# Kernel optimization log

Measured on AMD Instinct MI355X. Metric: run time of the kernel, lower is better.

## Reference

```python
import jax, jax.numpy as jnp
import numpy as np

M = 10000      # spans with antecedents
KMAX = 30      # max antecedents per span
N = 12000      # total candidate spans (rows of g_i)
GDIM = 512     # span embedding dim
DDIM, GEDIM, SDIM = 20, 20, 20  # distance / genre / speaker embed dims
HID = 150      # Score hidden dim
GIJ = 3 * GDIM + DDIM + GEDIM + SDIM  # 1596
NDIST, NGENRE, NSPK = 10, 7, 3


def setup_inputs() -> dict:
    rng = np.random.default_rng(0)
    lengths = rng.integers(1, KMAX + 1, size=M)           # antecedents per span
    P = int(lengths.sum())
    seg_ids = np.repeat(np.arange(1, M + 1), lengths).astype(np.int32)  # segment 0 is the leading empty split
    pos_in_seg = np.concatenate([np.arange(l) for l in lengths]).astype(np.int32)
    seg_lengths = np.concatenate([[0], lengths]).astype(np.int32)        # [S], S = M+1
    mention_ids = rng.integers(0, N, size=P).astype(np.int32)
    antecedent_ids = rng.integers(0, N, size=P).astype(np.int32)
    dist_idx = rng.integers(0, NDIST, size=P).astype(np.int32)
    genre_idx = rng.integers(0, NGENRE, size=P).astype(np.int32)
    speaker_idx = rng.integers(0, NSPK, size=P).astype(np.int32)

    ks = jax.random.split(jax.random.key(0), 12)
    sc = lambda d: 1.0 / np.sqrt(d)
    return {
        'g_i': jax.random.normal(ks[0], (N, GDIM), jnp.float32),
        'mention_scores': jax.random.normal(ks[1], (N, 1), jnp.float32),
        'dist_emb': jax.random.normal(ks[2], (NDIST, DDIM), jnp.float32),
        'genre_emb': jax.random.normal(ks[3], (NGENRE, GEDIM), jnp.float32),
        'speaker_emb': jax.random.normal(ks[4], (NSPK, SDIM), jnp.float32),
        'W1': jax.random.normal(ks[5], (GIJ, HID), jnp.float32) * sc(GIJ),
        'b1': jnp.zeros((HID,), jnp.float32),
        'W2': jax.random.normal(ks[6], (HID, HID), jnp.float32) * sc(HID),
        'b2': jnp.zeros((HID,), jnp.float32),
        'W3': jax.random.normal(ks[7], (HID, 1), jnp.float32) * sc(HID),
        'b3': jnp.zeros((1,), jnp.float32),
        'mention_ids': jnp.asarray(mention_ids),
        'antecedent_ids': jnp.asarray(antecedent_ids),
        'dist_idx': jnp.asarray(dist_idx),
        'genre_idx': jnp.asarray(genre_idx),
        'speaker_idx': jnp.asarray(speaker_idx),
        'seg_ids': jnp.asarray(seg_ids),
        'pos_in_seg': jnp.asarray(pos_in_seg),
        'seg_lengths': jnp.asarray(seg_lengths),
    }


def reference(g_i, mention_scores, dist_emb, genre_emb, speaker_emb,
              W1, b1, W2, b2, W3, b3,
              mention_ids, antecedent_ids, dist_idx, genre_idx, speaker_idx,
              seg_ids, pos_in_seg, seg_lengths):
    # phi = cat(distance, genre, speaker) side features, [P, 60]
    phi = jnp.concatenate([dist_emb[dist_idx], genre_emb[genre_idx], speaker_emb[speaker_idx]], axis=1)
    i_g = g_i[mention_ids]      # [P, GDIM] irregular gather
    j_g = g_i[antecedent_ids]   # [P, GDIM]
    pairs = jnp.concatenate([i_g, j_g, i_g * j_g, phi], axis=1)  # [P, GIJ]
    # 3-layer MLP scorer (dropout is identity at inference)
    h = jax.nn.relu(pairs @ W1 + b1)
    h = jax.nn.relu(h @ W2 + b2)
    s_ij = (h @ W3 + b3)[:, 0]  # [P]
    coref = mention_scores[mention_ids, 0] + mention_scores[antecedent_ids, 0] + s_ij  # [P]
    # variable-length segment softmax with epsilon=0 appended, padded with 1000
    S = seg_lengths.shape[0]
    dense = jnp.full((S, KMAX + 1), -jnp.inf, jnp.float32)
    dense = dense.at[seg_ids, pos_in_seg].set(coref)
    dense = dense.at[jnp.arange(S), seg_lengths].set(0.0)  # epsilon slot
    probs = jax.nn.softmax(dense, axis=1)  # -inf slots -> 0
    col = jnp.arange(KMAX + 1)
    probs = jnp.where(col[None, :] > seg_lengths[:, None], 1000.0, probs)  # pad value 1000
    return probs  # [S, KMAX+1]
```

## Files before the change

kernel.cpp:

```cpp
#include <hip/hip_runtime.h>
#include <stdint.h>

#define GDIM   512
#define HID    150
#define HIDP   160
#define NROWS  12000
#define KP1    31
#define BM     128

typedef __attribute__((ext_vector_type(4))) float f32x4;
typedef __attribute__((ext_vector_type(2))) float f32x2;
typedef long i64;

__device__ __forceinline__ unsigned short f2bf(float x){
    unsigned int u = __float_as_uint(x);
    return (unsigned short)((u + 0x7fffu + ((u >> 16) & 1u)) >> 16);
}
__device__ __forceinline__ float bf2f(unsigned short u){
    return __uint_as_float(((unsigned int)u) << 16);
}
__device__ __forceinline__ i64 u2l(uint2 v){ return __builtin_bit_cast(i64, v); }
__device__ __forceinline__ f32x4 mfma8(i64 a, i64 b, f32x4 c){
    return __builtin_amdgcn_mfma_f32_16x16x32_fp8_fp8(a, b, c, 0, 0, 0);
}
__device__ __forceinline__ uint2 f8mulpk(uint2 m, uint2 a){
    f32x2 m0 = __builtin_amdgcn_cvt_pk_f32_fp8(m.x, false);
    f32x2 m1 = __builtin_amdgcn_cvt_pk_f32_fp8(m.x, true);
    f32x2 m2 = __builtin_amdgcn_cvt_pk_f32_fp8(m.y, false);
    f32x2 m3 = __builtin_amdgcn_cvt_pk_f32_fp8(m.y, true);
    f32x2 a0 = __builtin_amdgcn_cvt_pk_f32_fp8(a.x, false);
    f32x2 a1 = __builtin_amdgcn_cvt_pk_f32_fp8(a.x, true);
    f32x2 a2 = __builtin_amdgcn_cvt_pk_f32_fp8(a.y, false);
    f32x2 a3 = __builtin_amdgcn_cvt_pk_f32_fp8(a.y, true);
    unsigned int r0 = 0, r1 = 0;
    r0 = __builtin_amdgcn_cvt_pk_fp8_f32(m0[0]*a0[0], m0[1]*a0[1], r0, false);
    r0 = __builtin_amdgcn_cvt_pk_fp8_f32(m1[0]*a1[0], m1[1]*a1[1], r0, true);
    r1 = __builtin_amdgcn_cvt_pk_fp8_f32(m2[0]*a2[0], m2[1]*a2[1], r1, false);
    r1 = __builtin_amdgcn_cvt_pk_fp8_f32(m3[0]*a3[0], m3[1]*a3[1], r1, true);
    return (uint2){r0, r1};
}
__device__ __forceinline__ void glds16(const void* g, void* l){
    __builtin_amdgcn_global_load_lds(
        (const __attribute__((address_space(1))) unsigned int*)g,
        (__attribute__((address_space(3))) unsigned int*)l, 16, 0, 0);
}

__global__ void k_prep0(const float* __restrict__ g, unsigned char* __restrict__ g8,
                        int* __restrict__ hist, int4* __restrict__ recs,
                        const float* __restrict__ W1, unsigned char* __restrict__ W18,
                        const float* __restrict__ W2, unsigned char* __restrict__ W28, int P){
    int i = blockIdx.x * blockDim.x + threadIdx.x;
    if (i < NROWS) hist[i] = 0;
    if (i < BM) recs[P + i] = (int4){0, 0, (int)0x80000000, 0};
    if (i < 30720){
        int s = i / 10240, r = i % 10240;
        int n = r >> 6, gi = r & 63;
        int gdst = gi ^ (n & 7);
        int k0 = s * 512 + gi * 8;
        float x[8];
        #pragma unroll
        for (int e = 0; e < 8; e++) x[e] = (n < HID) ? W1[(size_t)(k0 + e) * HID + n] : 0.f;
        unsigned int d0 = 0, d1 = 0;
        d0 = __builtin_amdgcn_cvt_pk_fp8_f32(x[0], x[1], d0, false);
        d0 = __builtin_amdgcn_cvt_pk_fp8_f32(x[2], x[3], d0, true);
        d1 = __builtin_amdgcn_cvt_pk_fp8_f32(x[4], x[5], d1, false);
        d1 = __builtin_amdgcn_cvt_pk_fp8_f32(x[6], x[7], d1, true);
        *reinterpret_cast<uint2*>(W18 + (size_t)s * 81920 + n * 512 + gdst * 8) = (uint2){d0, d1};
    }
    if (i < 6912){
        int n2 = i / 42, kd = (i % 42) * 4;
        float y[4];
        #pragma unroll
        for (int e = 0; e < 4; e++){
            int k = kd + e;
            y[e] = (n2 < HID && k < HID) ? W2[(size_t)k * HID + n2] : 0.f;
        }
        unsigned int d = 0;
        d = __builtin_amdgcn_cvt_pk_fp8_f32(y[0], y[1], d, false);
        d = __builtin_amdgcn_cvt_pk_fp8_f32(y[2], y[3], d, true);
        reinterpret_cast<unsigned int*>(W28)[i] = d;
    }
    if (i >= NROWS * 32) return;
    int lh = i & 3, kt = (i >> 2) & 7, row = i >> 5;
    const float* src = g + (size_t)row * 512 + kt * 64 + lh * 8;
    float4 x0 = *reinterpret_cast<const float4*>(src);
    float4 x1 = *reinterpret_cast<const float4*>(src + 4);
    float4 x2 = *reinterpret_cast<const float4*>(src + 32);
    float4 x3 = *reinterpret_cast<const float4*>(src + 36);
    uint4 o; unsigned int d;
    d = 0; d = __builtin_amdgcn_cvt_pk_fp8_f32(x0.x, x0.y, d, false);
    d = __builtin_amdgcn_cvt_pk_fp8_f32(x0.z, x0.w, d, true);  o.x = d;
    d = 0; d = __builtin_amdgcn_cvt_pk_fp8_f32(x1.x, x1.y, d, false);
    d = __builtin_amdgcn_cvt_pk_fp8_f32(x1.z, x1.w, d, true);  o.y = d;
    d = 0; d = __builtin_amdgcn_cvt_pk_fp8_f32(x2.x, x2.y, d, false);
    d = __builtin_amdgcn_cvt_pk_fp8_f32(x2.z, x2.w, d, true);  o.z = d;
    d = 0; d = __builtin_amdgcn_cvt_pk_fp8_f32(x3.x, x3.y, d, false);
    d = __builtin_amdgcn_cvt_pk_fp8_f32(x3.z, x3.w, d, true);  o.w = d;
    *reinterpret_cast<uint4*>(g8 + (size_t)row * 512 + kt * 64 + lh * 16) = o;
}

__global__ void k_wprep(const float* __restrict__ de, const float* __restrict__ ge,
                        const float* __restrict__ se, const float* __restrict__ W1,
                        const float* __restrict__ b1,
                        const float* __restrict__ W3, const float* __restrict__ b2,
                        unsigned short* __restrict__ PhiW,
                        float* __restrict__ w3p, float* __restrict__ b2p){
    int c = blockIdx.x, tid = threadIdx.x;
    if (c < 210 && tid < HIDP){
        int si = c % 3, gi2 = (c / 3) % 7, di = c / 21;
        float acc = 0.f;
        if (tid < HID){
            acc = b1[tid];
            #pragma unroll
            for (int dd = 0; dd < 20; dd++) acc += de[di*20 + dd] * W1[(size_t)(1536 + dd) * HID + tid];
            #pragma unroll
            for (int dd = 0; dd < 20; dd++) acc += ge[gi2*20 + dd] * W1[(size_t)(1556 + dd) * HID + tid];
            #pragma unroll
            for (int dd = 0; dd < 20; dd++) acc += se[si*20 + dd] * W1[(size_t)(1576 + dd) * HID + tid];
        }
        PhiW[c * HIDP + tid] = f2bf(acc);
    }
    if (c == 210 && tid < HIDP){
        w3p[tid] = (tid < HID) ? W3[tid] : 0.f;
        b2p[tid] = (tid < HID) ? b2[tid] : 0.f;
    }
}

__global__ void k_hist(const int* __restrict__ mid, int* __restrict__ hist, int P){
    int p = blockIdx.x * blockDim.x + threadIdx.x;
    if (p < P) atomicAdd(&hist[mid[p]], 1);
}
__global__ void k_scan(const int* __restrict__ hist, int* __restrict__ offsw, int nb){
    __shared__ int part[1024];
    int t = threadIdx.x;
    int chunk = (nb + 1023) / 1024;
    int lo = t * chunk, hi = lo + chunk; if (hi > nb) hi = nb;
    int s = 0;
    for (int b = lo; b < hi; b++) s += hist[b];
    part[t] = s;
    __syncthreads();
    for (int d = 1; d < 1024; d <<= 1){
        int v = (t >= d) ? part[t - d] : 0;
        __syncthreads();
        part[t] += v;
        __syncthreads();
    }
    int run = part[t] - s;
    for (int b = lo; b < hi; b++){ offsw[b] = run; run += hist[b]; }
}
__global__ void k_scatter(const int* __restrict__ mident, const int* __restrict__ antid,
                          const int* __restrict__ di, const int* __restrict__ gi, const int* __restrict__ si,
                          const int* __restrict__ seg, const int* __restrict__ pos, const float* __restrict__ ms,
                          int* __restrict__ offsw, int4* __restrict__ recs, int P){
    int p = blockIdx.x * blockDim.x + threadIdx.x;
    if (p >= P) return;
    int m = mident[p], a = antid[p];
    int idx = atomicAdd(&offsw[m], 1);
    int combo = (di[p] * 7 + gi[p]) * 3 + si[p];
    int meta = (combo << 19) | (seg[p] << 5) | pos[p];
    int4 r; r.x = m; r.y = a; r.z = meta; r.w = __float_as_int(ms[m] + ms[a]);
    recs[idx] = r;
}

__global__ __launch_bounds__(256) void k_proj(const unsigned char* __restrict__ g8,
                                              const unsigned char* __restrict__ W18,
                                              unsigned char* __restrict__ out){
    __shared__ __align__(16) char smem[81920];
    const unsigned char* Wt = W18 + (size_t)blockIdx.y * 81920;
    unsigned char* outh = out + (size_t)blockIdx.y * NROWS * HIDP;
    int tid = threadIdx.x, lane = tid & 63, w = tid >> 6;
    int l15 = lane & 15, lh = lane >> 4;
    int swz8 = (l15 & 7) << 3;
    int row0 = blockIdx.x * BM;

    int r0 = row0 + 32*w + l15;       int r0c = (r0 < NROWS) ? r0 : NROWS - 1;
    int r1 = r0 + 16;                 int r1c = (r1 < NROWS) ? r1 : NROWS - 1;
    const unsigned char* gp0 = g8 + (size_t)r0c * GDIM + lh * 16;
    const unsigned char* gp1 = g8 + (size_t)r1c * GDIM + lh * 16;

    #pragma unroll
    for (int i = 0; i < 20; i++){
        int c = w * 20 + i;
        glds16(Wt + c * 1024 + lane * 16, smem + c * 1024);
    }

    f32x4 acc1[10][2];
    #pragma unroll
    for (int t = 0; t < 10; t++){ acc1[t][0] = (f32x4){0,0,0,0}; acc1[t][1] = (f32x4){0,0,0,0}; }

    asm volatile("s_waitcnt vmcnt(0)" ::: "memory");
    __builtin_amdgcn_s_barrier();

    uint4 R0 = *reinterpret_cast<const uint4*>(gp0);
    uint4 R1 = *reinterpret_cast<const uint4*>(gp1);
    #pragma unroll
    for (int kt = 0; kt < 8; kt++){
        uint4 N0, N1;
        if (kt < 7){
            N0 = *reinterpret_cast<const uint4*>(gp0 + (kt+1)*64);
            N1 = *reinterpret_cast<const uint4*>(gp1 + (kt+1)*64);
        }
        i64 a00 = u2l((uint2){R0.x, R0.y}), a01 = u2l((uint2){R0.z, R0.w});
        i64 a10 = u2l((uint2){R1.x, R1.y}), a11 = u2l((uint2){R1.z, R1.w});
        #pragma unroll
        for (int t = 0; t < 10; t++){
            int rowb = (t*16 + l15) * 512;
            i64 b0 = *reinterpret_cast<const i64*>(&smem[rowb + ((kt*64 +  0 + lh*8) ^ swz8)]);
            i64 b1 = *reinterpret_cast<const i64*>(&smem[rowb + ((kt*64 + 32 + lh*8) ^ swz8)]);
            acc1[t][0] = mfma8(b0, a00, acc1[t][0]);
            acc1[t][1] = mfma8(b0, a10, acc1[t][1]);
            acc1[t][0] = mfma8(b1, a01, acc1[t][0]);
            acc1[t][1] = mfma8(b1, a11, acc1[t][1]);
        }
        R0 = N0; R1 = N1;
    }

    #pragma unroll
    for (int rf = 0; rf < 2; rf++){
        int row = row0 + 32*w + 16*rf + l15;
        if (row < NROWS){
            #pragma unroll
            for (int t = 0; t < 10; t++){
                f32x4 a = acc1[t][rf];
                unsigned int dw = 0;
                dw = __builtin_amdgcn_cvt_pk_fp8_f32(a[0], a[1], dw, false);
                dw = __builtin_amdgcn_cvt_pk_fp8_f32(a[2], a[3], dw, true);
                *reinterpret_cast<unsigned int*>(outh + (size_t)row * HIDP + 16*t + 4*lh) = dw;
            }
        }
    }
}

__global__ __launch_bounds__(256) void k_fused(
    const unsigned char* __restrict__ g8,
    const unsigned char* __restrict__ W1c8, const unsigned char* __restrict__ W28,
    const unsigned short* __restrict__ PhiW, const unsigned char* __restrict__ Am,
    const unsigned char* __restrict__ Aa,
    const float* __restrict__ w3p, const float* __restrict__ b2p, const float* __restrict__ b3,
    const int4* __restrict__ recs,
    float* __restrict__ dense)
{
    __shared__ __align__(16) char smem[81920];
    int tid = threadIdx.x, lane = tid & 63, w = tid >> 6;
    int l15 = lane & 15, lh = lane >> 4;
    int swz8 = (l15 & 7) << 3;
    int p0 = blockIdx.x * BM;

    int4 rec0 = recs[p0 + 32*w + l15];
    int4 rec1 = recs[p0 + 32*w + 16 + l15];

    const unsigned char* gm0 = g8 + (size_t)rec0.x * GDIM + lh * 16;
    const unsigned char* ga0 = g8 + (size_t)rec0.y * GDIM + lh * 16;
    const unsigned char* gm1 = g8 + (size_t)rec1.x * GDIM + lh * 16;
    const unsigned char* ga1 = g8 + (size_t)rec1.y * GDIM + lh * 16;

    #pragma unroll
    for (int i = 0; i < 20; i++){
        int c = w * 20 + i;
        glds16(W1c8 + c * 1024 + lane * 16, smem + c * 1024);
    }

    f32x4 acc1[10][2];
    #pragma unroll
    for (int t = 0; t < 10; t++){ acc1[t][0] = (f32x4){0,0,0,0}; acc1[t][1] = (f32x4){0,0,0,0}; }

    asm volatile("s_waitcnt vmcnt(0)" ::: "memory");
    __builtin_amdgcn_s_barrier();

    uint4 Rm0 = *reinterpret_cast<const uint4*>(gm0);
    uint4 Ra0 = *reinterpret_cast<const uint4*>(ga0);
    uint4 Rm1 = *reinterpret_cast<const uint4*>(gm1);
    uint4 Ra1 = *reinterpret_cast<const uint4*>(ga1);
    #pragma unroll
    for (int kt = 0; kt < 8; kt++){
        uint4 Nm0, Na0, Nm1, Na1;
        if (kt < 7){
            Nm0 = *reinterpret_cast<const uint4*>(gm0 + (kt+1)*64);
            Na0 = *reinterpret_cast<const uint4*>(ga0 + (kt+1)*64);
            Nm1 = *reinterpret_cast<const uint4*>(gm1 + (kt+1)*64);
            Na1 = *reinterpret_cast<const uint4*>(ga1 + (kt+1)*64);
        }
        uint2 p00 = f8mulpk((uint2){Rm0.x, Rm0.y}, (uint2){Ra0.x, Ra0.y});
        uint2 p01 = f8mulpk((uint2){Rm0.z, Rm0.w}, (uint2){Ra0.z, Ra0.w});
        uint2 p10 = f8mulpk((uint2){Rm1.x, Rm1.y}, (uint2){Ra1.x, Ra1.y});
        uint2 p11 = f8mulpk((uint2){Rm1.z, Rm1.w}, (uint2){Ra1.z, Ra1.w});
        i64 lp00 = u2l(p00), lp01 = u2l(p01), lp10 = u2l(p10), lp11 = u2l(p11);
        #pragma unroll
        for (int t = 0; t < 10; t++){
            int rowb = (t*16 + l15) * 512;
            i64 b0 = *reinterpret_cast<const i64*>(&smem[rowb + ((kt*64 +  0 + lh*8) ^ swz8)]);
            i64 b1 = *reinterpret_cast<const i64*>(&smem[rowb + ((kt*64 + 32 + lh*8) ^ swz8)]);
            acc1[t][0] = mfma8(b0, lp00, acc1[t][0]);
            acc1[t][1] = mfma8(b0, lp10, acc1[t][1]);
            acc1[t][0] = mfma8(b1, lp01, acc1[t][0]);
            acc1[t][1] = mfma8(b1, lp11, acc1[t][1]);
        }
        Rm0 = Nm0; Ra0 = Na0; Rm1 = Nm1; Ra1 = Na1;
    }

    asm volatile("s_waitcnt lgkmcnt(0)" ::: "memory");
    __builtin_amdgcn_s_barrier();

    #pragma unroll
    for (int i = 0; i < 7; i++){
        int c = w * 7 + i;
        if (c < 27) glds16(W28 + c * 1024 + lane * 16, smem + 21504 + c * 1024);
    }

    #pragma unroll
    for (int rf = 0; rf < 2; rf++){
        int4 rc = rf ? rec1 : rec0;
        int pr = 32*w + 16*rf + l15;
        const unsigned char* amp = Am + (size_t)rc.x * HIDP;
        const unsigned char* aap = Aa + (size_t)rc.y * HIDP;
        int combo = (rc.z >> 19) & 0xFF;
        const unsigned short* php = PhiW + (size_t)combo * HIDP;
        char* h1row = smem + pr * 168;
        #pragma unroll
        for (int t = 0; t < 10; t++){
            int h0 = 16*t + 4*lh;
            unsigned int amd = *reinterpret_cast<const unsigned int*>(amp + h0);
            unsigned int aad = *reinterpret_cast<const unsigned int*>(aap + h0);
            ushort4 ph4 = *reinterpret_cast<const ushort4*>(php + h0);
            f32x2 amL = __builtin_amdgcn_cvt_pk_f32_fp8(amd, false);
            f32x2 amH = __builtin_amdgcn_cvt_pk_f32_fp8(amd, true);
            f32x2 aaL = __builtin_amdgcn_cvt_pk_f32_fp8(aad, false);
            f32x2 aaH = __builtin_amdgcn_cvt_pk_f32_fp8(aad, true);
            f32x4 a = acc1[t][rf];
            float v0 = fmaxf(a[0] + amL[0] + aaL[0] + bf2f(ph4.x), 0.f);
            float v1 = fmaxf(a[1] + amL[1] + aaL[1] + bf2f(ph4.y), 0.f);
            float v2 = fmaxf(a[2] + amH[0] + aaH[0] + bf2f(ph4.z), 0.f);
            float v3 = fmaxf(a[3] + amH[1] + aaH[1] + bf2f(ph4.w), 0.f);
            unsigned int dw = 0;
            dw = __builtin_amdgcn_cvt_pk_fp8_f32(v0, v1, dw, false);
            dw = __builtin_amdgcn_cvt_pk_fp8_f32(v2, v3, dw, true);
            *reinterpret_cast<unsigned int*>(h1row + h0) = dw;
        }
    }

    asm volatile("s_waitcnt vmcnt(0) lgkmcnt(0)" ::: "memory");
    __builtin_amdgcn_s_barrier();

    f32x4 acc2[10][2];
    #pragma unroll
    for (int t = 0; t < 10; t++){ acc2[t][0] = (f32x4){0,0,0,0}; acc2[t][1] = (f32x4){0,0,0,0}; }
    const char* w2b = smem + 21504;
    #pragma unroll
    for (int k2 = 0; k2 < 5; k2++){
        i64 h0f = *reinterpret_cast<const i64*>(smem + (32*w + l15)      * 168 + k2*32 + lh*8);
        i64 h1f = *reinterpret_cast<const i64*>(smem + (32*w + 16 + l15) * 168 + k2*32 + lh*8);
        #pragma unroll
        for (int t = 0; t < 10; t++){
            i64 wf = *reinterpret_cast<const i64*>(w2b + (16*t + l15) * 168 + k2*32 + lh*8);
            acc2[t][0] = mfma8(wf, h0f, acc2[t][0]);
            acc2[t][1] = mfma8(wf, h1f, acc2[t][1]);
        }
    }

    float b3v = b3[0];
    #pragma unroll
    for (int rf = 0; rf < 2; rf++){
        int4 rc = rf ? rec1 : rec0;
        float s = 0.f;
        #pragma unroll
        for (int t = 0; t < 10; t++){
            f32x4 w3v = *reinterpret_cast<const f32x4*>(w3p + 16*t + 4*lh);
            f32x4 b2v = *reinterpret_cast<const f32x4*>(b2p + 16*t + 4*lh);
            f32x4 a = acc2[t][rf];
            s += fmaxf(a[0] + b2v[0], 0.f) * w3v[0];
            s += fmaxf(a[1] + b2v[1], 0.f) * w3v[1];
            s += fmaxf(a[2] + b2v[2], 0.f) * w3v[2];
            s += fmaxf(a[3] + b2v[3], 0.f) * w3v[3];
        }
        s += __shfl_xor(s, 16);
        s += __shfl_xor(s, 32);
        if (!(rc.z & 0x80000000) && lh == 0){
            float val = s + b3v + __int_as_float(rc.w);
            dense[(size_t)((rc.z >> 5) & 0x3FFF) * KP1 + (rc.z & 31)] = val;
        }
    }
}

__global__ void k_softmax(const float* __restrict__ dense, const int* __restrict__ seg_lengths,
                          float* __restrict__ out, int S){
    int wid = threadIdx.x >> 6, lane = threadIdx.x & 63;
    int s = blockIdx.x * 4 + wid;
    if (s >= S) return;
    int len = seg_lengths[s];
    float ninf = -__builtin_inff();
    float val = ninf;
    if (lane < KP1) val = (lane < len) ? dense[(size_t)s * KP1 + lane] : ((lane == len) ? 0.f : ninf);
    float m = val;
    #pragma unroll
    for (int msk = 1; msk < 64; msk <<= 1) m = fmaxf(m, __shfl_xor(m, msk));
    float e = expf(val - m);
    float sum = e;
    #pragma unroll
    for (int msk = 1; msk < 64; msk <<= 1) sum += __shfl_xor(sum, msk);
    if (lane < KP1) out[(size_t)s * KP1 + lane] = (lane > len) ? 1000.f : (e / sum);
}

extern "C" void kernel_launch(void* const* d_in, const int* in_sizes, int n_in,
                              void* d_out, int out_size, void* d_ws, size_t ws_size,
                              hipStream_t stream){
    const float* g_i        = (const float*)d_in[0];
    const float* ms         = (const float*)d_in[1];
    const float* dist_emb   = (const float*)d_in[2];
    const float* genre_emb  = (const float*)d_in[3];
    const float* spk_emb    = (const float*)d_in[4];
    const float* W1         = (const float*)d_in[5];
    const float* b1         = (const float*)d_in[6];
    const float* W2         = (const float*)d_in[7];
    const float* b2         = (const float*)d_in[8];
    const float* W3         = (const float*)d_in[9];
    const float* b3         = (const float*)d_in[10];
    const int* mention_ids  = (const int*)d_in[11];
    const int* antecedent_ids = (const int*)d_in[12];
    const int* dist_idx     = (const int*)d_in[13];
    const int* genre_idx    = (const int*)d_in[14];
    const int* spk_idx      = (const int*)d_in[15];
    const int* seg_ids      = (const int*)d_in[16];
    const int* pos_in_seg   = (const int*)d_in[17];
    const int* seg_lengths  = (const int*)d_in[18];
    int P = in_sizes[11];
    int S = in_sizes[18];

    char* ws = (char*)d_ws;
    unsigned char* W18   = (unsigned char*)(ws + 0);
    unsigned char* W28   = (unsigned char*)(ws + 245760);
    unsigned short* PhiW = (unsigned short*)(ws + 273408);
    float* w3pad         = (float*)(ws + 340608);
    float* b2pad         = (float*)(ws + 341248);
    unsigned char* g8    = (unsigned char*)(ws + 341888);
    unsigned char* Am8   = (unsigned char*)(ws + 6485888);
    unsigned char* Aa8   = (unsigned char*)(ws + 8405888);
    int* hist            = (int*)(ws + 10325888);
    int* offsw           = (int*)(ws + 10373888);
    int4* recs           = (int4*)(ws + 10421888);
    float* dense         = (float*)(ws + 13000192);

    k_prep0<<<1500, 256, 0, stream>>>(g_i, g8, hist, recs, W1, W18, W2, W28, P);
    k_wprep<<<211, 256, 0, stream>>>(dist_emb, genre_emb, spk_emb, W1, b1, W3, b2,
                                     PhiW, w3pad, b2pad);
    k_hist<<<(P + 255)/256, 256, 0, stream>>>(mention_ids, hist, P);
    k_scan<<<1, 1024, 0, stream>>>(hist, offsw, NROWS);
    k_scatter<<<(P + 255)/256, 256, 0, stream>>>(mention_ids, antecedent_ids, dist_idx, genre_idx,
        spk_idx, seg_ids, pos_in_seg, ms, offsw, recs, P);

    k_proj<<<dim3((NROWS + BM - 1)/BM, 2), 256, 0, stream>>>(g8, W18, Am8);

    k_fused<<<(P + BM - 1)/BM, 256, 0, stream>>>(g8, W18 + 2*81920, W28, PhiW,
        Am8, Aa8, w3pad, b2pad, b3, recs, dense);

    k_softmax<<<(S + 3)/4, 256, 0, stream>>>(dense, seg_lengths, (float*)d_out, S);
}
```

Measured before the change: 116.3 us.

## Merge weight-prep kernel into prep0, add MFMA priority hints and XCD block remap

```diff
diff --git a/kernel.cpp b/kernel.cpp
--- a/kernel.cpp
+++ b/kernel.cpp
@@ -6,7 +6,8 @@
 #define HIDP   160
 #define NROWS  12000
 #define KP1    31
-#define BM     128
+#define BMP    128
+#define BMF    128
 
 typedef __attribute__((ext_vector_type(4))) float f32x4;
 typedef __attribute__((ext_vector_type(2))) float f32x2;
@@ -48,10 +49,15 @@
 __global__ void k_prep0(const float* __restrict__ g, unsigned char* __restrict__ g8,
                         int* __restrict__ hist, int4* __restrict__ recs,
                         const float* __restrict__ W1, unsigned char* __restrict__ W18,
-                        const float* __restrict__ W2, unsigned char* __restrict__ W28, int P){
+                        const float* __restrict__ W2, unsigned char* __restrict__ W28,
+                        const float* __restrict__ de, const float* __restrict__ ge,
+                        const float* __restrict__ se, const float* __restrict__ b1,
+                        const float* __restrict__ W3, const float* __restrict__ b2,
+                        unsigned short* __restrict__ PhiW,
+                        float* __restrict__ w3p, float* __restrict__ b2p, int P){
     int i = blockIdx.x * blockDim.x + threadIdx.x;
     if (i < NROWS) hist[i] = 0;
-    if (i < BM) recs[P + i] = (int4){0, 0, (int)0x80000000, 0};
+    if (i < BMF) recs[P + i] = (int4){0, 0, (int)0x80000000, 0};
     if (i < 30720){
         int s = i / 10240, r = i % 10240;
         int n = r >> 6, gi = r & 63;
@@ -80,49 +86,42 @@
         d = __builtin_amdgcn_cvt_pk_fp8_f32(y[2], y[3], d, true);
         reinterpret_cast<unsigned int*>(W28)[i] = d;
     }
-    if (i >= NROWS * 32) return;
-    int lh = i & 3, kt = (i >> 2) & 7, row = i >> 5;
-    const float* src = g + (size_t)row * 512 + kt * 64 + lh * 8;
-    float4 x0 = *reinterpret_cast<const float4*>(src);
-    float4 x1 = *reinterpret_cast<const float4*>(src + 4);
-    float4 x2 = *reinterpret_cast<const float4*>(src + 32);
-    float4 x3 = *reinterpret_cast<const float4*>(src + 36);
-    uint4 o; unsigned int d;
-    d = 0; d = __builtin_amdgcn_cvt_pk_fp8_f32(x0.x, x0.y, d, false);
-    d = __builtin_amdgcn_cvt_pk_fp8_f32(x0.z, x0.w, d, true);  o.x = d;
-    d = 0; d = __builtin_amdgcn_cvt_pk_fp8_f32(x1.x, x1.y, d, false);
-    d = __builtin_amdgcn_cvt_pk_fp8_f32(x1.z, x1.w, d, true);  o.y = d;
-    d = 0; d = __builtin_amdgcn_cvt_pk_fp8_f32(x2.x, x2.y, d, false);
-    d = __builtin_amdgcn_cvt_pk_fp8_f32(x2.z, x2.w, d, true);  o.z = d;
-    d = 0; d = __builtin_amdgcn_cvt_pk_fp8_f32(x3.x, x3.y, d, false);
-    d = __builtin_amdgcn_cvt_pk_fp8_f32(x3.z, x3.w, d, true);  o.w = d;
-    *reinterpret_cast<uint4*>(g8 + (size_t)row * 512 + kt * 64 + lh * 16) = o;
-}
-
-__global__ void k_wprep(const float* __restrict__ de, const float* __restrict__ ge,
-                        const float* __restrict__ se, const float* __restrict__ W1,
-                        const float* __restrict__ b1,
-                        const float* __restrict__ W3, const float* __restrict__ b2,
-                        unsigned short* __restrict__ PhiW,
-                        float* __restrict__ w3p, float* __restrict__ b2p){
-    int c = blockIdx.x, tid = threadIdx.x;
-    if (c < 210 && tid < HIDP){
+    if (i < NROWS * 32){
+        int lh = i & 3, kt = (i >> 2) & 7, row = i >> 5;
+        const float* src = g + (size_t)row * 512 + kt * 64 + lh * 8;
+        float4 x0 = *reinterpret_cast<const float4*>(src);
+        float4 x1 = *reinterpret_cast<const float4*>(src + 4);
+        float4 x2 = *reinterpret_cast<const float4*>(src + 32);
+        float4 x3 = *reinterpret_cast<const float4*>(src + 36);
+        uint4 o; unsigned int d;
+        d = 0; d = __builtin_amdgcn_cvt_pk_fp8_f32(x0.x, x0.y, d, false);
+        d = __builtin_amdgcn_cvt_pk_fp8_f32(x0.z, x0.w, d, true);  o.x = d;
+        d = 0; d = __builtin_amdgcn_cvt_pk_fp8_f32(x1.x, x1.y, d, false);
+        d = __builtin_amdgcn_cvt_pk_fp8_f32(x1.z, x1.w, d, true);  o.y = d;
+        d = 0; d = __builtin_amdgcn_cvt_pk_fp8_f32(x2.x, x2.y, d, false);
+        d = __builtin_amdgcn_cvt_pk_fp8_f32(x2.z, x2.w, d, true);  o.z = d;
+        d = 0; d = __builtin_amdgcn_cvt_pk_fp8_f32(x3.x, x3.y, d, false);
+        d = __builtin_amdgcn_cvt_pk_fp8_f32(x3.z, x3.w, d, true);  o.w = d;
+        *reinterpret_cast<uint4*>(g8 + (size_t)row * 512 + kt * 64 + lh * 16) = o;
+    } else if (i < NROWS * 32 + 33600){
+        int j = i - NROWS * 32;
+        int c = j / HIDP, h = j - c * HIDP;
         int si = c % 3, gi2 = (c / 3) % 7, di = c / 21;
         float acc = 0.f;
-        if (tid < HID){
-            acc = b1[tid];
+        if (h < HID){
+            acc = b1[h];
             #pragma unroll
-            for (int dd = 0; dd < 20; dd++) acc += de[di*20 + dd] * W1[(size_t)(1536 + dd) * HID + tid];
+            for (int dd = 0; dd < 20; dd++) acc += de[di*20 + dd] * W1[(size_t)(1536 + dd) * HID + h];
             #pragma unroll
-            for (int dd = 0; dd < 20; dd++) acc += ge[gi2*20 + dd] * W1[(size_t)(1556 + dd) * HID + tid];
+            for (int dd = 0; dd < 20; dd++) acc += ge[gi2*20 + dd] * W1[(size_t)(1556 + dd) * HID + h];
             #pragma unroll
-            for (int dd = 0; dd < 20; dd++) acc += se[si*20 + dd] * W1[(size_t)(1576 + dd) * HID + tid];
-        }
-        PhiW[c * HIDP + tid] = f2bf(acc);
-    }
-    if (c == 210 && tid < HIDP){
-        w3p[tid] = (tid < HID) ? W3[tid] : 0.f;
-        b2p[tid] = (tid < HID) ? b2[tid] : 0.f;
+            for (int dd = 0; dd < 20; dd++) acc += se[si*20 + dd] * W1[(size_t)(1576 + dd) * HID + h];
+        }
+        PhiW[c * HIDP + h] = f2bf(acc);
+    } else if (i < NROWS * 32 + 33600 + HIDP){
+        int h = i - NROWS * 32 - 33600;
+        w3p[h] = (h < HID) ? W3[h] : 0.f;
+        b2p[h] = (h < HID) ? b2[h] : 0.f;
     }
 }
 
@@ -171,7 +170,7 @@
     int tid = threadIdx.x, lane = tid & 63, w = tid >> 6;
     int l15 = lane & 15, lh = lane >> 4;
     int swz8 = (l15 & 7) << 3;
-    int row0 = blockIdx.x * BM;
+    int row0 = blockIdx.x * BMP;
 
     int r0 = row0 + 32*w + l15;       int r0c = (r0 < NROWS) ? r0 : NROWS - 1;
     int r1 = r0 + 16;                 int r1c = (r1 < NROWS) ? r1 : NROWS - 1;
@@ -202,6 +201,7 @@
         }
         i64 a00 = u2l((uint2){R0.x, R0.y}), a01 = u2l((uint2){R0.z, R0.w});
         i64 a10 = u2l((uint2){R1.x, R1.y}), a11 = u2l((uint2){R1.z, R1.w});
+        __builtin_amdgcn_s_setprio(1);
         #pragma unroll
         for (int t = 0; t < 10; t++){
             int rowb = (t*16 + l15) * 512;
@@ -212,6 +212,7 @@
             acc1[t][0] = mfma8(b1, a01, acc1[t][0]);
             acc1[t][1] = mfma8(b1, a11, acc1[t][1]);
         }
+        __builtin_amdgcn_s_setprio(0);
         R0 = N0; R1 = N1;
     }
 
@@ -244,7 +245,14 @@
     int tid = threadIdx.x, lane = tid & 63, w = tid >> 6;
     int l15 = lane & 15, lh = lane >> 4;
     int swz8 = (l15 & 7) << 3;
-    int p0 = blockIdx.x * BM;
+
+    int nwg = gridDim.x, orig = blockIdx.x, bid = orig;
+    if (nwg >= 8){
+        int q = nwg >> 3, r = nwg & 7;
+        int xcd = orig & 7, lid = orig >> 3;
+        bid = (xcd < r ? xcd * (q + 1) : r * (q + 1) + (xcd - r) * q) + lid;
+    }
+    int p0 = bid * BMF;
 
     int4 rec0 = recs[p0 + 32*w + l15];
     int4 rec1 = recs[p0 + 32*w + 16 + l15];
@@ -285,6 +293,7 @@
         uint2 p10 = f8mulpk((uint2){Rm1.x, Rm1.y}, (uint2){Ra1.x, Ra1.y});
         uint2 p11 = f8mulpk((uint2){Rm1.z, Rm1.w}, (uint2){Ra1.z, Ra1.w});
         i64 lp00 = u2l(p00), lp01 = u2l(p01), lp10 = u2l(p10), lp11 = u2l(p11);
+        __builtin_amdgcn_s_setprio(1);
         #pragma unroll
         for (int t = 0; t < 10; t++){
             int rowb = (t*16 + l15) * 512;
@@ -295,6 +304,7 @@
             acc1[t][0] = mfma8(b1, lp01, acc1[t][0]);
             acc1[t][1] = mfma8(b1, lp11, acc1[t][1]);
         }
+        __builtin_amdgcn_s_setprio(0);
         Rm0 = Nm0; Ra0 = Na0; Rm1 = Nm1; Ra1 = Na1;
     }
 
@@ -345,6 +355,7 @@
     #pragma unroll
     for (int t = 0; t < 10; t++){ acc2[t][0] = (f32x4){0,0,0,0}; acc2[t][1] = (f32x4){0,0,0,0}; }
     const char* w2b = smem + 21504;
+    __builtin_amdgcn_s_setprio(1);
     #pragma unroll
     for (int k2 = 0; k2 < 5; k2++){
         i64 h0f = *reinterpret_cast<const i64*>(smem + (32*w + l15)      * 168 + k2*32 + lh*8);
@@ -356,6 +367,7 @@
             acc2[t][1] = mfma8(wf, h1f, acc2[t][1]);
         }
     }
+    __builtin_amdgcn_s_setprio(0);
 
     float b3v = b3[0];
     #pragma unroll
@@ -439,17 +451,17 @@
     int4* recs           = (int4*)(ws + 10421888);
     float* dense         = (float*)(ws + 13000192);
 
-    k_prep0<<<1500, 256, 0, stream>>>(g_i, g8, hist, recs, W1, W18, W2, W28, P);
-    k_wprep<<<211, 256, 0, stream>>>(dist_emb, genre_emb, spk_emb, W1, b1, W3, b2,
-                                     PhiW, w3pad, b2pad);
+    int prep_threads = NROWS * 32 + 33600 + HIDP;
+    k_prep0<<<(prep_threads + 255)/256, 256, 0, stream>>>(g_i, g8, hist, recs, W1, W18, W2, W28,
+        dist_emb, genre_emb, spk_emb, b1, W3, b2, PhiW, w3pad, b2pad, P);
     k_hist<<<(P + 255)/256, 256, 0, stream>>>(mention_ids, hist, P);
     k_scan<<<1, 1024, 0, stream>>>(hist, offsw, NROWS);
     k_scatter<<<(P + 255)/256, 256, 0, stream>>>(mention_ids, antecedent_ids, dist_idx, genre_idx,
         spk_idx, seg_ids, pos_in_seg, ms, offsw, recs, P);
 
-    k_proj<<<dim3((NROWS + BM - 1)/BM, 2), 256, 0, stream>>>(g8, W18, Am8);
-
-    k_fused<<<(P + BM - 1)/BM, 256, 0, stream>>>(g8, W18 + 2*81920, W28, PhiW,
+    k_proj<<<dim3((NROWS + BMP - 1)/BMP, 2), 256, 0, stream>>>(g8, W18, Am8);
+
+    k_fused<<<(P + BMF - 1)/BMF, 256, 0, stream>>>(g8, W18 + 2*81920, W28, PhiW,
         Am8, Aa8, w3pad, b2pad, b3, recs, dense);
 
     k_softmax<<<(S + 3)/4, 256, 0, stream>>>(dense, seg_lengths, (float*)d_out, S);
```

Result: faster. 111.4 us (-4.2%).
